# Performance work log

Hardware: AMD Instinct MI355X
Metric: run time of the kernel (lower is better)

The kernel has to match this reference:

```python
import jax, jax.numpy as jnp
import numpy as np

B, C, H, W = 4, 512, 64, 64
DQ = C // 8  # 64


def _conv1x1(x, w, b):
    # x: [B,C,H,W], w: [O,C], b: [O] -> [B,O,H,W]
    return jnp.einsum('bchw,oc->bohw', x, w) + b[None, :, None, None]


def setup_inputs() -> dict:
    key = jax.random.key(0)
    ks = jax.random.split(key, 12)
    s = 0.02  # conv weight init scale
    inp = {
        'x1': jax.random.normal(ks[0], (B, C, H, W), jnp.float32),
        'x2': jax.random.normal(ks[1], (B, C, H, W), jnp.float32),
        'wq1': jax.random.normal(ks[2], (DQ, C), jnp.float32) * s,
        'bq1': jnp.zeros((DQ,), jnp.float32),
        'wk1': jax.random.normal(ks[3], (DQ, C), jnp.float32) * s,
        'bk1': jnp.zeros((DQ,), jnp.float32),
        'wv1': jax.random.normal(ks[4], (C, C), jnp.float32) * s,
        'bv1': jnp.zeros((C,), jnp.float32),
        'wq2': jax.random.normal(ks[5], (DQ, C), jnp.float32) * s,
        'bq2': jnp.zeros((DQ,), jnp.float32),
        'wk2': jax.random.normal(ks[6], (DQ, C), jnp.float32) * s,
        'bk2': jnp.zeros((DQ,), jnp.float32),
        'wv2': jax.random.normal(ks[7], (C, C), jnp.float32) * s,
        'bv2': jnp.zeros((C,), jnp.float32),
        'gamma1': jax.random.normal(ks[8], (1,), jnp.float32) * 0.1,
        'gamma2': jax.random.normal(ks[9], (1,), jnp.float32) * 0.1,
    }
    return inp


def reference(x1, x2, wq1, bq1, wk1, bk1, wv1, bv1,
              wq2, bq2, wk2, bk2, wv2, bv2, gamma1, gamma2):
    b, c, h, w = x1.shape
    n = h * w
    # 1x1-conv projections, flattened to token axis n = h*w
    q1 = _conv1x1(x1, wq1, bq1).reshape(b, -1, n)  # [B,DQ,N]
    k1 = _conv1x1(x1, wk1, bk1).reshape(b, -1, n)  # [B,DQ,N]
    v1 = _conv1x1(x1, wv1, bv1).reshape(b, c, n)   # [B,C,N]
    q2 = _conv1x1(x2, wq2, bq2).reshape(b, -1, n)
    k2 = _conv1x1(x2, wk2, bk2).reshape(b, -1, n)
    v2 = _conv1x1(x2, wv2, bv2).reshape(b, c, n)

    # cross attention 1: queries from x1, keys/values from x2 (no 1/sqrt(d) scaling, per source)
    att1 = jax.nn.softmax(jnp.einsum('bdn,bdm->bnm', q1, k2), axis=-1)  # [B,N,N]
    out1 = jnp.einsum('bcn,bmn->bcm', v2, att1).reshape(b, c, h, w)

    # cross attention 2: queries from x2, keys/values from x1
    att2 = jax.nn.softmax(jnp.einsum('bdn,bdm->bnm', q2, k1), axis=-1)  # [B,N,N]
    out2 = jnp.einsum('bcn,bmn->bcm', v1, att2).reshape(b, c, h, w)

    out1 = x1 + gamma1 * out1
    out2 = x2 + gamma2 * out2
    return out1, out2
```

## Files before the change

### kernel.cpp

```cpp
#include <hip/hip_runtime.h>
#include <hip/hip_bf16.h>

#define NT 4096
#define CD 512
#define DQV 64
#define NB 4

typedef float f32x4 __attribute__((ext_vector_type(4)));
typedef short bf16x8 __attribute__((ext_vector_type(8)));

__device__ __forceinline__ short f2bf(float x){
  union { __hip_bfloat16 b; short s; } u;
  u.b = __float2bfloat16(x);
  return u.s;
}

__global__ void cast_weights(const float* __restrict__ wq1, const float* __restrict__ wk1,
                             const float* __restrict__ wv1, const float* __restrict__ wq2,
                             const float* __restrict__ wk2, const float* __restrict__ wv2,
                             short* __restrict__ out){
  int id = blockIdx.x * 256 + threadIdx.x;
  if (id >= 655360) return;
  float v;
  if (id < 32768)        v = wq1[id];
  else if (id < 65536)   v = wk1[id - 32768];
  else if (id < 327680)  v = wv1[id - 65536];
  else if (id < 360448)  v = wq2[id - 327680];
  else if (id < 393216)  v = wk2[id - 360448];
  else                   v = wv2[id - 393216];
  out[id] = f2bf(v);
}

__global__ void transpose_cast(const float* __restrict__ x1, const float* __restrict__ x2,
                               short* __restrict__ XT1, short* __restrict__ XT2){
  __shared__ short t[64][66];
  int nt = blockIdx.x, ct = blockIdx.y, z = blockIdx.z;
  int b = z & 3, inp = z >> 2;
  const float* xb = (inp ? x2 : x1) + (size_t)b * CD * NT;
  short* xtb = (inp ? XT2 : XT1) + (size_t)b * NT * CD;
  int n0 = nt * 64, c0 = ct * 64;
  int tid = threadIdx.x;
  int nl = tid & 63, cl0 = (tid >> 6) * 2;
#pragma unroll
  for (int cc = 0; cc < 8; ++cc){
    int c = cl0 + cc * 8;
    float v0 = xb[(size_t)(c0 + c) * NT + n0 + nl];
    float v1 = xb[(size_t)(c0 + c + 1) * NT + n0 + nl];
    union { unsigned u; short s[2]; } p;
    p.s[0] = f2bf(v0); p.s[1] = f2bf(v1);
    *(unsigned*)&t[nl][c] = p.u;
  }
  __syncthreads();
  int cl = (tid & 31) * 2, nl0 = tid >> 5;
#pragma unroll
  for (int nn = 0; nn < 8; ++nn){
    int n = nl0 + nn * 8;
    *(unsigned*)&xtb[(size_t)(n0 + n) * CD + c0 + cl] = *(const unsigned*)&t[n][cl];
  }
}

__global__ void proj_qk(const short* __restrict__ XT1, const short* __restrict__ XT2,
                        const short* __restrict__ WB,
                        const float* __restrict__ bq1, const float* __restrict__ bk1,
                        const float* __restrict__ bq2, const float* __restrict__ bk2,
                        short* __restrict__ Q1, short* __restrict__ K1,
                        short* __restrict__ Q2, short* __restrict__ K2){
  int pt = blockIdx.y;
  const short* xt = (pt < 2) ? XT1 : XT2;
  const short* w  = WB + (pt == 0 ? 0 : pt == 1 ? 32768 : pt == 2 ? 327680 : 360448);
  const float* bias = (pt == 0) ? bq1 : (pt == 1) ? bk1 : (pt == 2) ? bq2 : bk2;
  short* out = (pt == 0) ? Q1 : (pt == 1) ? K1 : (pt == 2) ? Q2 : K2;
  int row0 = blockIdx.x * 128;
  int wid = threadIdx.x >> 6, lane = threadIdx.x & 63;
  int lr = lane & 15, lk = (lane >> 4) * 8, lq4 = (lane >> 4) * 4;
  f32x4 acc[2][4] = {};
#pragma unroll 2
  for (int kk = 0; kk < 16; ++kk){
    int k0 = kk * 32 + lk;
    bf16x8 a[2], bb[4];
#pragma unroll
    for (int fr = 0; fr < 2; ++fr)
      a[fr] = *(const bf16x8*)&xt[(size_t)(row0 + wid*32 + fr*16 + lr) * CD + k0];
#pragma unroll
    for (int fc = 0; fc < 4; ++fc)
      bb[fc] = *(const bf16x8*)&w[(size_t)(fc*16 + lr) * CD + k0];
#pragma unroll
    for (int fr = 0; fr < 2; ++fr)
#pragma unroll
      for (int fc = 0; fc < 4; ++fc)
        acc[fr][fc] = __builtin_amdgcn_mfma_f32_16x16x32_bf16(a[fr], bb[fc], acc[fr][fc], 0,0,0);
  }
#pragma unroll
  for (int fr = 0; fr < 2; ++fr)
#pragma unroll
    for (int fc = 0; fc < 4; ++fc){
      int col = fc*16 + lr;
      float bsv = bias[col];
#pragma unroll
      for (int r = 0; r < 4; ++r){
        int row = row0 + wid*32 + fr*16 + lq4 + r;
        out[(size_t)row * DQV + col] = f2bf(acc[fr][fc][r] + bsv);
      }
    }
}

__global__ void proj_v(const short* __restrict__ XT1, const short* __restrict__ XT2,
                       const short* __restrict__ WB,
                       const float* __restrict__ bv1, const float* __restrict__ bv2,
                       short* __restrict__ V1, short* __restrict__ V2){
  int inp = blockIdx.z, b = blockIdx.y;
  int ct = blockIdx.x >> 6, nt = blockIdx.x & 63;
  const short* xt = (inp ? XT2 : XT1) + (size_t)b * NT * CD;
  const short* w  = WB + (inp ? 393216 : 65536);
  const float* bias = inp ? bv2 : bv1;
  short* V = (inp ? V2 : V1) + (size_t)b * CD * NT;
  int c0 = ct * 128, n0 = nt * 64;
  int wid = threadIdx.x >> 6, lane = threadIdx.x & 63;
  int ch = wid >> 1, nh = wid & 1;
  int lr = lane & 15, lk = (lane >> 4) * 8, lq4 = (lane >> 4) * 4;
  f32x4 acc[4][2] = {};
#pragma unroll 2
  for (int kk = 0; kk < 16; ++kk){
    int k0 = kk * 32 + lk;
    bf16x8 a[4], bb[2];
#pragma unroll
    for (int fr = 0; fr < 4; ++fr)
      a[fr] = *(const bf16x8*)&w[(size_t)(c0 + ch*64 + fr*16 + lr) * CD + k0];
#pragma unroll
    for (int fc = 0; fc < 2; ++fc)
      bb[fc] = *(const bf16x8*)&xt[(size_t)(n0 + nh*32 + fc*16 + lr) * CD + k0];
#pragma unroll
    for (int fr = 0; fr < 4; ++fr)
#pragma unroll
      for (int fc = 0; fc < 2; ++fc)
        acc[fr][fc] = __builtin_amdgcn_mfma_f32_16x16x32_bf16(a[fr], bb[fc], acc[fr][fc], 0,0,0);
  }
#pragma unroll
  for (int fr = 0; fr < 4; ++fr)
#pragma unroll
    for (int fc = 0; fc < 2; ++fc)
#pragma unroll
      for (int r = 0; r < 4; ++r){
        int c = c0 + ch*64 + fr*16 + lq4 + r;
        int n = n0 + nh*32 + fc*16 + lr;
        V[(size_t)c * NT + n] = f2bf(acc[fr][fc][r] + bias[c]);
      }
}

__global__ void __launch_bounds__(512, 4) attn_fused(
    const short* __restrict__ Q1, const short* __restrict__ K1, const short* __restrict__ V1,
    const short* __restrict__ Q2, const short* __restrict__ K2, const short* __restrict__ V2,
    const float* __restrict__ x1, const float* __restrict__ x2,
    const float* __restrict__ g1, const float* __restrict__ g2,
    float* __restrict__ out){
  __shared__ float S[64][68];
  __shared__ __align__(16) short P[64][72];
  __shared__ float lrow[64], crow[64];

  int bid = blockIdx.x;
  int pair = bid & 7, qb = bid >> 3;
  int b = pair & 3, at = pair >> 2;
  const short* Q = at ? Q2 : Q1;
  const short* K = at ? K1 : K2;
  const short* V = at ? V1 : V2;
  const float* xr = at ? x2 : x1;
  float gamma = at ? g2[0] : g1[0];
  float* outp = out + (size_t)at * NB*CD*NT + (size_t)b * CD*NT;
  const float* xrb = xr + (size_t)b * CD*NT;
  const short* Qb = Q + ((size_t)b*NT + (size_t)qb*64) * DQV;
  const short* Kb = K + (size_t)b*NT*DQV;
  const short* Vb = V + (size_t)b*CD*NT;

  int tid = threadIdx.x, wid = tid >> 6, lane = tid & 63;
  int lr = lane & 15, lk8 = (lane >> 4) * 8, lq4 = (lane >> 4) * 4;

  int ih = wid >> 2, jq = wid & 3;
  bf16x8 qf[2][2];
#pragma unroll
  for (int fr = 0; fr < 2; ++fr)
#pragma unroll
    for (int fk = 0; fk < 2; ++fk)
      qf[fr][fk] = *(const bf16x8*)&Qb[(size_t)(ih*32 + fr*16 + lr) * DQV + fk*32 + lk8];

  f32x4 acc[4][4] = {};
  int c0 = wid * 64;
  int si = tid >> 3, sj = (tid & 7) * 8;
  float m_reg = -1e30f, l_reg = 0.f;

#pragma unroll 1
  for (int jt = 0; jt < 64; ++jt){
    int j0 = jt * 64;
    f32x4 s0 = {}, s1 = {};
#pragma unroll
    for (int fk = 0; fk < 2; ++fk){
      bf16x8 kf = *(const bf16x8*)&Kb[(size_t)(j0 + jq*16 + lr) * DQV + fk*32 + lk8];
      s0 = __builtin_amdgcn_mfma_f32_16x16x32_bf16(qf[0][fk], kf, s0, 0,0,0);
      s1 = __builtin_amdgcn_mfma_f32_16x16x32_bf16(qf[1][fk], kf, s1, 0,0,0);
    }
#pragma unroll
    for (int r = 0; r < 4; ++r){
      S[ih*32 + lq4 + r][jq*16 + lr]      = s0[r];
      S[ih*32 + 16 + lq4 + r][jq*16 + lr] = s1[r];
    }
    __syncthreads();
    {
      f32x4 sa = *(const f32x4*)&S[si][sj];
      f32x4 sb = *(const f32x4*)&S[si][sj + 4];
      float mx = fmaxf(fmaxf(fmaxf(sa[0], sa[1]), fmaxf(sa[2], sa[3])),
                       fmaxf(fmaxf(sb[0], sb[1]), fmaxf(sb[2], sb[3])));
      mx = fmaxf(mx, __shfl_xor(mx, 1));
      mx = fmaxf(mx, __shfl_xor(mx, 2));
      mx = fmaxf(mx, __shfl_xor(mx, 4));
      float mn = fmaxf(m_reg, mx);
      float cf = __expf(m_reg - mn);
      float e0 = __expf(sa[0] - mn), e1 = __expf(sa[1] - mn);
      float e2 = __expf(sa[2] - mn), e3 = __expf(sa[3] - mn);
      float e4 = __expf(sb[0] - mn), e5 = __expf(sb[1] - mn);
      float e6 = __expf(sb[2] - mn), e7 = __expf(sb[3] - mn);
      float sum = ((e0 + e1) + (e2 + e3)) + ((e4 + e5) + (e6 + e7));
      bf16x8 pv;
      pv[0] = f2bf(e0); pv[1] = f2bf(e1); pv[2] = f2bf(e2); pv[3] = f2bf(e3);
      pv[4] = f2bf(e4); pv[5] = f2bf(e5); pv[6] = f2bf(e6); pv[7] = f2bf(e7);
      *(bf16x8*)&P[si][sj] = pv;
      sum += __shfl_xor(sum, 1);
      sum += __shfl_xor(sum, 2);
      sum += __shfl_xor(sum, 4);
      l_reg = l_reg * cf + sum;
      m_reg = mn;
      if ((tid & 7) == 0) crow[si] = cf;
    }
    __syncthreads();
    {
      float cf0 = crow[lr], cf1 = crow[16 + lr], cf2 = crow[32 + lr], cf3 = crow[48 + lr];
      bool ident = (cf0 == 1.f) & (cf1 == 1.f) & (cf2 == 1.f) & (cf3 == 1.f);
      if (!__all(ident)){
        float cfa[4] = {cf0, cf1, cf2, cf3};
#pragma unroll
        for (int ci = 0; ci < 4; ++ci){
          float cf = cfa[ci];
#pragma unroll
          for (int cr = 0; cr < 4; ++cr){
            acc[cr][ci][0] *= cf; acc[cr][ci][1] *= cf;
            acc[cr][ci][2] *= cf; acc[cr][ci][3] *= cf;
          }
        }
      }
    }
#pragma unroll
    for (int kk = 0; kk < 2; ++kk){
      bf16x8 pf[4];
#pragma unroll
      for (int ci = 0; ci < 4; ++ci)
        pf[ci] = *(const bf16x8*)&P[ci*16 + lr][kk*32 + lk8];
#pragma unroll
      for (int cr = 0; cr < 4; ++cr){
        bf16x8 vf = *(const bf16x8*)&Vb[(size_t)(c0 + cr*16 + lr) * NT + j0 + kk*32 + lk8];
#pragma unroll
        for (int ci = 0; ci < 4; ++ci)
          acc[cr][ci] = __builtin_amdgcn_mfma_f32_16x16x32_bf16(vf, pf[ci], acc[cr][ci], 0,0,0);
      }
    }
    __syncthreads();
  }
  if ((tid & 7) == 0) lrow[si] = l_reg;
  __syncthreads();
#pragma unroll
  for (int ci = 0; ci < 4; ++ci){
    float linv = 1.f / lrow[ci*16 + lr];
    int ig = qb*64 + ci*16 + lr;
#pragma unroll
    for (int cr = 0; cr < 4; ++cr)
#pragma unroll
      for (int r = 0; r < 4; ++r){
        int c = c0 + cr*16 + lq4 + r;
        size_t idx = (size_t)c * NT + ig;
        outp[idx] = xrb[idx] + gamma * acc[cr][ci][r] * linv;
      }
  }
}

extern "C" void kernel_launch(void* const* d_in, const int* in_sizes, int n_in,
                              void* d_out, int out_size, void* d_ws, size_t ws_size,
                              hipStream_t stream) {
  const float* x1  = (const float*)d_in[0];
  const float* x2  = (const float*)d_in[1];
  const float* wq1 = (const float*)d_in[2];
  const float* bq1 = (const float*)d_in[3];
  const float* wk1 = (const float*)d_in[4];
  const float* bk1 = (const float*)d_in[5];
  const float* wv1 = (const float*)d_in[6];
  const float* bv1 = (const float*)d_in[7];
  const float* wq2 = (const float*)d_in[8];
  const float* bq2 = (const float*)d_in[9];
  const float* wk2 = (const float*)d_in[10];
  const float* bk2 = (const float*)d_in[11];
  const float* wv2 = (const float*)d_in[12];
  const float* bv2 = (const float*)d_in[13];
  const float* g1  = (const float*)d_in[14];
  const float* g2  = (const float*)d_in[15];

  short* XT1 = (short*)d_ws;
  short* XT2 = XT1 + 8388608;
  short* Q1  = XT2 + 8388608;
  short* K1  = Q1 + 1048576;
  short* Q2  = K1 + 1048576;
  short* K2  = Q2 + 1048576;
  short* V1  = K2 + 1048576;
  short* V2  = V1 + 8388608;
  short* WB  = V2 + 8388608;

  cast_weights<<<2560, 256, 0, stream>>>(wq1, wk1, wv1, wq2, wk2, wv2, WB);
  transpose_cast<<<dim3(64, 8, 8), 256, 0, stream>>>(x1, x2, XT1, XT2);
  proj_qk<<<dim3(128, 4), 256, 0, stream>>>(XT1, XT2, WB, bq1, bk1, bq2, bk2, Q1, K1, Q2, K2);
  proj_v<<<dim3(256, 4, 2), 256, 0, stream>>>(XT1, XT2, WB, bv1, bv2, V1, V2);
  attn_fused<<<512, 512, 0, stream>>>(Q1, K1, V1, Q2, K2, V2, x1, x2, g1, g2, (float*)d_out);
}
```

Measured before the change: 646.8 us.

## Halve attention query tile to 32 rows, prefetch K/V, raise occupancy

The fused attention kernel now handles 32 query rows per block instead of 64 and launches twice as many blocks, with launch bounds raised to allow more resident blocks. K fragments for the next tile are prefetched, V fragments are loaded before the QK MFMA, and the PV MFMA section runs at raised wave priority. The trailing per-iteration barrier is removed, which is safe because shared-memory reuse is already ordered by the next iteration's barriers. The aim is more parallelism and better latency hiding. The cost is that each V tile is reused by half as many queries, roughly doubling V reads, and the tighter register budget may cause spills.

```diff
diff --git a/kernel.cpp b/kernel.cpp
--- a/kernel.cpp
+++ b/kernel.cpp
@@ -8,6 +8,7 @@
 
 typedef float f32x4 __attribute__((ext_vector_type(4)));
 typedef short bf16x8 __attribute__((ext_vector_type(8)));
+typedef short bf16x4 __attribute__((ext_vector_type(4)));
 
 __device__ __forceinline__ short f2bf(float x){
   union { __hip_bfloat16 b; short s; } u;
@@ -147,15 +148,15 @@
       }
 }
 
-__global__ void __launch_bounds__(512, 4) attn_fused(
+__global__ void __launch_bounds__(512, 8) attn_fused(
     const short* __restrict__ Q1, const short* __restrict__ K1, const short* __restrict__ V1,
     const short* __restrict__ Q2, const short* __restrict__ K2, const short* __restrict__ V2,
     const float* __restrict__ x1, const float* __restrict__ x2,
     const float* __restrict__ g1, const float* __restrict__ g2,
     float* __restrict__ out){
-  __shared__ float S[64][68];
-  __shared__ __align__(16) short P[64][72];
-  __shared__ float lrow[64], crow[64];
+  __shared__ float S[32][69];
+  __shared__ __align__(16) short P[32][80];
+  __shared__ float lrow[32], crow[32];
 
   int bid = blockIdx.x;
   int pair = bid & 7, qb = bid >> 3;
@@ -167,107 +168,103 @@
   float gamma = at ? g2[0] : g1[0];
   float* outp = out + (size_t)at * NB*CD*NT + (size_t)b * CD*NT;
   const float* xrb = xr + (size_t)b * CD*NT;
-  const short* Qb = Q + ((size_t)b*NT + (size_t)qb*64) * DQV;
+  const short* Qb = Q + ((size_t)b*NT + (size_t)qb*32) * DQV;
   const short* Kb = K + (size_t)b*NT*DQV;
   const short* Vb = V + (size_t)b*CD*NT;
 
   int tid = threadIdx.x, wid = tid >> 6, lane = tid & 63;
   int lr = lane & 15, lk8 = (lane >> 4) * 8, lq4 = (lane >> 4) * 4;
 
-  int ih = wid >> 2, jq = wid & 3;
-  bf16x8 qf[2][2];
-#pragma unroll
-  for (int fr = 0; fr < 2; ++fr)
-#pragma unroll
-    for (int fk = 0; fk < 2; ++fk)
-      qf[fr][fk] = *(const bf16x8*)&Qb[(size_t)(ih*32 + fr*16 + lr) * DQV + fk*32 + lk8];
-
-  f32x4 acc[4][4] = {};
+  int rh = wid >> 2, cb = wid & 3;
+  bf16x8 qf[2];
+#pragma unroll
+  for (int fk = 0; fk < 2; ++fk)
+    qf[fk] = *(const bf16x8*)&Qb[(size_t)(rh*16 + lr) * DQV + fk*32 + lk8];
+
+  f32x4 acc[4][2] = {};
   int c0 = wid * 64;
-  int si = tid >> 3, sj = (tid & 7) * 8;
+  int si = tid >> 4, sj = (tid & 15) * 4;
   float m_reg = -1e30f, l_reg = 0.f;
+
+  bf16x8 kf0 = *(const bf16x8*)&Kb[(size_t)(cb*16 + lr) * DQV + lk8];
+  bf16x8 kf1 = *(const bf16x8*)&Kb[(size_t)(cb*16 + lr) * DQV + 32 + lk8];
 
 #pragma unroll 1
   for (int jt = 0; jt < 64; ++jt){
     int j0 = jt * 64;
-    f32x4 s0 = {}, s1 = {};
-#pragma unroll
-    for (int fk = 0; fk < 2; ++fk){
-      bf16x8 kf = *(const bf16x8*)&Kb[(size_t)(j0 + jq*16 + lr) * DQV + fk*32 + lk8];
-      s0 = __builtin_amdgcn_mfma_f32_16x16x32_bf16(qf[0][fk], kf, s0, 0,0,0);
-      s1 = __builtin_amdgcn_mfma_f32_16x16x32_bf16(qf[1][fk], kf, s1, 0,0,0);
-    }
-#pragma unroll
-    for (int r = 0; r < 4; ++r){
-      S[ih*32 + lq4 + r][jq*16 + lr]      = s0[r];
-      S[ih*32 + 16 + lq4 + r][jq*16 + lr] = s1[r];
-    }
+    bf16x8 vf[4][2];
+#pragma unroll
+    for (int cr = 0; cr < 4; ++cr)
+#pragma unroll
+      for (int kk = 0; kk < 2; ++kk)
+        vf[cr][kk] = *(const bf16x8*)&Vb[(size_t)(c0 + cr*16 + lr) * NT + j0 + kk*32 + lk8];
+    f32x4 s0 = {};
+    s0 = __builtin_amdgcn_mfma_f32_16x16x32_bf16(qf[0], kf0, s0, 0,0,0);
+    s0 = __builtin_amdgcn_mfma_f32_16x16x32_bf16(qf[1], kf1, s0, 0,0,0);
+    if (jt < 63){
+      kf0 = *(const bf16x8*)&Kb[(size_t)(j0 + 64 + cb*16 + lr) * DQV + lk8];
+      kf1 = *(const bf16x8*)&Kb[(size_t)(j0 + 64 + cb*16 + lr) * DQV + 32 + lk8];
+    }
+#pragma unroll
+    for (int r = 0; r < 4; ++r)
+      S[rh*16 + lq4 + r][cb*16 + lr] = s0[r];
     __syncthreads();
     {
-      f32x4 sa = *(const f32x4*)&S[si][sj];
-      f32x4 sb = *(const f32x4*)&S[si][sj + 4];
-      float mx = fmaxf(fmaxf(fmaxf(sa[0], sa[1]), fmaxf(sa[2], sa[3])),
-                       fmaxf(fmaxf(sb[0], sb[1]), fmaxf(sb[2], sb[3])));
+      float v0 = S[si][sj], v1 = S[si][sj+1], v2 = S[si][sj+2], v3 = S[si][sj+3];
+      float mx = fmaxf(fmaxf(v0, v1), fmaxf(v2, v3));
       mx = fmaxf(mx, __shfl_xor(mx, 1));
       mx = fmaxf(mx, __shfl_xor(mx, 2));
       mx = fmaxf(mx, __shfl_xor(mx, 4));
+      mx = fmaxf(mx, __shfl_xor(mx, 8));
       float mn = fmaxf(m_reg, mx);
       float cf = __expf(m_reg - mn);
-      float e0 = __expf(sa[0] - mn), e1 = __expf(sa[1] - mn);
-      float e2 = __expf(sa[2] - mn), e3 = __expf(sa[3] - mn);
-      float e4 = __expf(sb[0] - mn), e5 = __expf(sb[1] - mn);
-      float e6 = __expf(sb[2] - mn), e7 = __expf(sb[3] - mn);
-      float sum = ((e0 + e1) + (e2 + e3)) + ((e4 + e5) + (e6 + e7));
-      bf16x8 pv;
+      float e0 = __expf(v0 - mn), e1 = __expf(v1 - mn);
+      float e2 = __expf(v2 - mn), e3 = __expf(v3 - mn);
+      float sum = (e0 + e1) + (e2 + e3);
+      bf16x4 pv;
       pv[0] = f2bf(e0); pv[1] = f2bf(e1); pv[2] = f2bf(e2); pv[3] = f2bf(e3);
-      pv[4] = f2bf(e4); pv[5] = f2bf(e5); pv[6] = f2bf(e6); pv[7] = f2bf(e7);
-      *(bf16x8*)&P[si][sj] = pv;
+      *(bf16x4*)&P[si][sj] = pv;
       sum += __shfl_xor(sum, 1);
       sum += __shfl_xor(sum, 2);
       sum += __shfl_xor(sum, 4);
+      sum += __shfl_xor(sum, 8);
       l_reg = l_reg * cf + sum;
       m_reg = mn;
-      if ((tid & 7) == 0) crow[si] = cf;
+      if ((tid & 15) == 0) crow[si] = cf;
     }
     __syncthreads();
     {
-      float cf0 = crow[lr], cf1 = crow[16 + lr], cf2 = crow[32 + lr], cf3 = crow[48 + lr];
-      bool ident = (cf0 == 1.f) & (cf1 == 1.f) & (cf2 == 1.f) & (cf3 == 1.f);
+      float cf0 = crow[lr], cf1 = crow[16 + lr];
+      bool ident = (cf0 == 1.f) & (cf1 == 1.f);
       if (!__all(ident)){
-        float cfa[4] = {cf0, cf1, cf2, cf3};
-#pragma unroll
-        for (int ci = 0; ci < 4; ++ci){
-          float cf = cfa[ci];
-#pragma unroll
-          for (int cr = 0; cr < 4; ++cr){
-            acc[cr][ci][0] *= cf; acc[cr][ci][1] *= cf;
-            acc[cr][ci][2] *= cf; acc[cr][ci][3] *= cf;
-          }
+#pragma unroll
+        for (int cr = 0; cr < 4; ++cr){
+          acc[cr][0][0] *= cf0; acc[cr][0][1] *= cf0; acc[cr][0][2] *= cf0; acc[cr][0][3] *= cf0;
+          acc[cr][1][0] *= cf1; acc[cr][1][1] *= cf1; acc[cr][1][2] *= cf1; acc[cr][1][3] *= cf1;
         }
       }
     }
+    __builtin_amdgcn_s_setprio(1);
 #pragma unroll
     for (int kk = 0; kk < 2; ++kk){
-      bf16x8 pf[4];
-#pragma unroll
-      for (int ci = 0; ci < 4; ++ci)
+      bf16x8 pf[2];
+#pragma unroll
+      for (int ci = 0; ci < 2; ++ci)
         pf[ci] = *(const bf16x8*)&P[ci*16 + lr][kk*32 + lk8];
 #pragma unroll
-      for (int cr = 0; cr < 4; ++cr){
-        bf16x8 vf = *(const bf16x8*)&Vb[(size_t)(c0 + cr*16 + lr) * NT + j0 + kk*32 + lk8];
-#pragma unroll
-        for (int ci = 0; ci < 4; ++ci)
-          acc[cr][ci] = __builtin_amdgcn_mfma_f32_16x16x32_bf16(vf, pf[ci], acc[cr][ci], 0,0,0);
-      }
-    }
-    __syncthreads();
-  }
-  if ((tid & 7) == 0) lrow[si] = l_reg;
+      for (int cr = 0; cr < 4; ++cr)
+#pragma unroll
+        for (int ci = 0; ci < 2; ++ci)
+          acc[cr][ci] = __builtin_amdgcn_mfma_f32_16x16x32_bf16(vf[cr][kk], pf[ci], acc[cr][ci], 0,0,0);
+    }
+    __builtin_amdgcn_s_setprio(0);
+  }
+  if ((tid & 15) == 0) lrow[si] = l_reg;
   __syncthreads();
 #pragma unroll
-  for (int ci = 0; ci < 4; ++ci){
+  for (int ci = 0; ci < 2; ++ci){
     float linv = 1.f / lrow[ci*16 + lr];
-    int ig = qb*64 + ci*16 + lr;
+    int ig = qb*32 + ci*16 + lr;
 #pragma unroll
     for (int cr = 0; cr < 4; ++cr)
 #pragma unroll
@@ -313,5 +310,5 @@
   transpose_cast<<<dim3(64, 8, 8), 256, 0, stream>>>(x1, x2, XT1, XT2);
   proj_qk<<<dim3(128, 4), 256, 0, stream>>>(XT1, XT2, WB, bq1, bk1, bq2, bk2, Q1, K1, Q2, K2);
   proj_v<<<dim3(256, 4, 2), 256, 0, stream>>>(XT1, XT2, WB, bv1, bv2, V1, V2);
-  attn_fused<<<512, 512, 0, stream>>>(Q1, K1, V1, Q2, K2, V2, x1, x2, g1, g2, (float*)d_out);
-}
+  attn_fused<<<1024, 512, 0, stream>>>(Q1, K1, V1, Q2, K2, V2, x1, x2, g1, g2, (float*)d_out);
+}
```

After: 1.821 ms. 2.82x slower.

## Widen attention key tile to 128, drop trailing barrier, raise PV priority

Applied to the files above, without the earlier changes.

The key/value tile in the fused flash-attention loop grows from 64 to 128 columns. This halves the loop trip count and the number of softmax rescale and barrier rounds, and each wave now computes a 32x32 block of S. The end-of-iteration __syncthreads is removed, relying on the next iteration's first barrier to protect the S, P and crow buffers. s_setprio raises wave priority around the PV MFMA section. The larger S and P shared buffers roughly double LDS use per block, which may lower the number of resident blocks per CU.

```diff
diff --git a/kernel.cpp b/kernel.cpp
--- a/kernel.cpp
+++ b/kernel.cpp
@@ -153,8 +153,8 @@
     const float* __restrict__ x1, const float* __restrict__ x2,
     const float* __restrict__ g1, const float* __restrict__ g2,
     float* __restrict__ out){
-  __shared__ float S[64][68];
-  __shared__ __align__(16) short P[64][72];
+  __shared__ float S[64][132];
+  __shared__ __align__(16) short P[64][136];
   __shared__ float lrow[64], crow[64];
 
   int bid = blockIdx.x;
@@ -174,54 +174,78 @@
   int tid = threadIdx.x, wid = tid >> 6, lane = tid & 63;
   int lr = lane & 15, lk8 = (lane >> 4) * 8, lq4 = (lane >> 4) * 4;
 
-  int ih = wid >> 2, jq = wid & 3;
+  int rh = wid >> 2, cb = wid & 3;
   bf16x8 qf[2][2];
 #pragma unroll
   for (int fr = 0; fr < 2; ++fr)
 #pragma unroll
     for (int fk = 0; fk < 2; ++fk)
-      qf[fr][fk] = *(const bf16x8*)&Qb[(size_t)(ih*32 + fr*16 + lr) * DQV + fk*32 + lk8];
+      qf[fr][fk] = *(const bf16x8*)&Qb[(size_t)(rh*32 + fr*16 + lr) * DQV + fk*32 + lk8];
 
   f32x4 acc[4][4] = {};
   int c0 = wid * 64;
-  int si = tid >> 3, sj = (tid & 7) * 8;
+  int si = tid >> 3, sj = (tid & 7) * 16;
   float m_reg = -1e30f, l_reg = 0.f;
 
 #pragma unroll 1
-  for (int jt = 0; jt < 64; ++jt){
-    int j0 = jt * 64;
-    f32x4 s0 = {}, s1 = {};
-#pragma unroll
-    for (int fk = 0; fk < 2; ++fk){
-      bf16x8 kf = *(const bf16x8*)&Kb[(size_t)(j0 + jq*16 + lr) * DQV + fk*32 + lk8];
-      s0 = __builtin_amdgcn_mfma_f32_16x16x32_bf16(qf[0][fk], kf, s0, 0,0,0);
-      s1 = __builtin_amdgcn_mfma_f32_16x16x32_bf16(qf[1][fk], kf, s1, 0,0,0);
-    }
-#pragma unroll
-    for (int r = 0; r < 4; ++r){
-      S[ih*32 + lq4 + r][jq*16 + lr]      = s0[r];
-      S[ih*32 + 16 + lq4 + r][jq*16 + lr] = s1[r];
-    }
+  for (int jt = 0; jt < 32; ++jt){
+    int j0 = jt * 128;
+    f32x4 s[2][2] = {};
+    bf16x8 kf[2][2];
+#pragma unroll
+    for (int fc = 0; fc < 2; ++fc)
+#pragma unroll
+      for (int fk = 0; fk < 2; ++fk)
+        kf[fc][fk] = *(const bf16x8*)&Kb[(size_t)(j0 + cb*32 + fc*16 + lr) * DQV + fk*32 + lk8];
+#pragma unroll
+    for (int fr = 0; fr < 2; ++fr)
+#pragma unroll
+      for (int fc = 0; fc < 2; ++fc){
+        s[fr][fc] = __builtin_amdgcn_mfma_f32_16x16x32_bf16(qf[fr][0], kf[fc][0], s[fr][fc], 0,0,0);
+        s[fr][fc] = __builtin_amdgcn_mfma_f32_16x16x32_bf16(qf[fr][1], kf[fc][1], s[fr][fc], 0,0,0);
+      }
+#pragma unroll
+    for (int fr = 0; fr < 2; ++fr)
+#pragma unroll
+      for (int fc = 0; fc < 2; ++fc)
+#pragma unroll
+        for (int r = 0; r < 4; ++r)
+          S[rh*32 + fr*16 + lq4 + r][cb*32 + fc*16 + lr] = s[fr][fc][r];
     __syncthreads();
     {
-      f32x4 sa = *(const f32x4*)&S[si][sj];
-      f32x4 sb = *(const f32x4*)&S[si][sj + 4];
-      float mx = fmaxf(fmaxf(fmaxf(sa[0], sa[1]), fmaxf(sa[2], sa[3])),
-                       fmaxf(fmaxf(sb[0], sb[1]), fmaxf(sb[2], sb[3])));
+      f32x4 a0 = *(const f32x4*)&S[si][sj];
+      f32x4 a1 = *(const f32x4*)&S[si][sj + 4];
+      f32x4 a2 = *(const f32x4*)&S[si][sj + 8];
+      f32x4 a3 = *(const f32x4*)&S[si][sj + 12];
+      float mx = fmaxf(fmaxf(fmaxf(a0[0],a0[1]),fmaxf(a0[2],a0[3])),
+                       fmaxf(fmaxf(a1[0],a1[1]),fmaxf(a1[2],a1[3])));
+      mx = fmaxf(mx, fmaxf(fmaxf(fmaxf(a2[0],a2[1]),fmaxf(a2[2],a2[3])),
+                           fmaxf(fmaxf(a3[0],a3[1]),fmaxf(a3[2],a3[3]))));
       mx = fmaxf(mx, __shfl_xor(mx, 1));
       mx = fmaxf(mx, __shfl_xor(mx, 2));
       mx = fmaxf(mx, __shfl_xor(mx, 4));
       float mn = fmaxf(m_reg, mx);
       float cf = __expf(m_reg - mn);
-      float e0 = __expf(sa[0] - mn), e1 = __expf(sa[1] - mn);
-      float e2 = __expf(sa[2] - mn), e3 = __expf(sa[3] - mn);
-      float e4 = __expf(sb[0] - mn), e5 = __expf(sb[1] - mn);
-      float e6 = __expf(sb[2] - mn), e7 = __expf(sb[3] - mn);
-      float sum = ((e0 + e1) + (e2 + e3)) + ((e4 + e5) + (e6 + e7));
-      bf16x8 pv;
-      pv[0] = f2bf(e0); pv[1] = f2bf(e1); pv[2] = f2bf(e2); pv[3] = f2bf(e3);
-      pv[4] = f2bf(e4); pv[5] = f2bf(e5); pv[6] = f2bf(e6); pv[7] = f2bf(e7);
-      *(bf16x8*)&P[si][sj] = pv;
+      bf16x8 p0, p1;
+      float sum = 0.f;
+#pragma unroll
+      for (int t = 0; t < 4; ++t){
+        float e = __expf(a0[t] - mn); sum += e; p0[t] = f2bf(e);
+      }
+#pragma unroll
+      for (int t = 0; t < 4; ++t){
+        float e = __expf(a1[t] - mn); sum += e; p0[4+t] = f2bf(e);
+      }
+#pragma unroll
+      for (int t = 0; t < 4; ++t){
+        float e = __expf(a2[t] - mn); sum += e; p1[t] = f2bf(e);
+      }
+#pragma unroll
+      for (int t = 0; t < 4; ++t){
+        float e = __expf(a3[t] - mn); sum += e; p1[4+t] = f2bf(e);
+      }
+      *(bf16x8*)&P[si][sj]     = p0;
+      *(bf16x8*)&P[si][sj + 8] = p1;
       sum += __shfl_xor(sum, 1);
       sum += __shfl_xor(sum, 2);
       sum += __shfl_xor(sum, 4);
@@ -231,10 +255,11 @@
     }
     __syncthreads();
     {
-      float cf0 = crow[lr], cf1 = crow[16 + lr], cf2 = crow[32 + lr], cf3 = crow[48 + lr];
-      bool ident = (cf0 == 1.f) & (cf1 == 1.f) & (cf2 == 1.f) & (cf3 == 1.f);
+      float cfa[4];
+#pragma unroll
+      for (int ci = 0; ci < 4; ++ci) cfa[ci] = crow[ci*16 + lr];
+      bool ident = (cfa[0] == 1.f) & (cfa[1] == 1.f) & (cfa[2] == 1.f) & (cfa[3] == 1.f);
       if (!__all(ident)){
-        float cfa[4] = {cf0, cf1, cf2, cf3};
 #pragma unroll
         for (int ci = 0; ci < 4; ++ci){
           float cf = cfa[ci];
@@ -246,8 +271,9 @@
         }
       }
     }
-#pragma unroll
-    for (int kk = 0; kk < 2; ++kk){
+    __builtin_amdgcn_s_setprio(1);
+#pragma unroll
+    for (int kk = 0; kk < 4; ++kk){
       bf16x8 pf[4];
 #pragma unroll
       for (int ci = 0; ci < 4; ++ci)
@@ -260,7 +286,7 @@
           acc[cr][ci] = __builtin_amdgcn_mfma_f32_16x16x32_bf16(vf, pf[ci], acc[cr][ci], 0,0,0);
       }
     }
-    __syncthreads();
+    __builtin_amdgcn_s_setprio(0);
   }
   if ((tid & 7) == 0) lrow[si] = l_reg;
   __syncthreads();
```

Result: slower. 776.2 us (+20.0%).

## Split attention channels across two blocks, prefetch V, and trim barriers

Applied to the files above, without the earlier changes.

The fused attention kernel now splits the 512 output channels into two halves handled by separate blocks, so the grid doubles to 1024. Each block's accumulator array halves, which lowers register pressure. The cost is that every block recomputes QK^T and the softmax for its query tile. V fragments are loaded at the top of each key-tile iteration, so the global loads overlap with the score and softmax work. The trailing per-iteration __syncthreads is removed, the remaining barriers use a lighter LDS-only wait, and wave priority is raised around the PV MFMA section.

```diff
diff --git a/kernel.cpp b/kernel.cpp
--- a/kernel.cpp
+++ b/kernel.cpp
@@ -14,6 +14,10 @@
   u.b = __float2bfloat16(x);
   return u.s;
 }
+
+#define BAR() do { asm volatile("s_waitcnt lgkmcnt(0)" ::: "memory"); \
+                   __builtin_amdgcn_s_barrier(); \
+                   asm volatile("" ::: "memory"); } while(0)
 
 __global__ void cast_weights(const float* __restrict__ wq1, const float* __restrict__ wk1,
                              const float* __restrict__ wv1, const float* __restrict__ wq2,
@@ -158,7 +162,9 @@
   __shared__ float lrow[64], crow[64];
 
   int bid = blockIdx.x;
-  int pair = bid & 7, qb = bid >> 3;
+  int pair = bid & 7;
+  int rest = bid >> 3;
+  int chalf = rest & 1, qb = rest >> 1;
   int b = pair & 3, at = pair >> 2;
   const short* Q = at ? Q2 : Q1;
   const short* K = at ? K1 : K2;
@@ -182,14 +188,20 @@
     for (int fk = 0; fk < 2; ++fk)
       qf[fr][fk] = *(const bf16x8*)&Qb[(size_t)(ih*32 + fr*16 + lr) * DQV + fk*32 + lk8];
 
-  f32x4 acc[4][4] = {};
-  int c0 = wid * 64;
+  f32x4 acc[2][4] = {};
+  int c0 = chalf * 256 + wid * 32;
   int si = tid >> 3, sj = (tid & 7) * 8;
   float m_reg = -1e30f, l_reg = 0.f;
 
 #pragma unroll 1
   for (int jt = 0; jt < 64; ++jt){
     int j0 = jt * 64;
+    bf16x8 vf[2][2];
+#pragma unroll
+    for (int cr = 0; cr < 2; ++cr)
+#pragma unroll
+      for (int kk = 0; kk < 2; ++kk)
+        vf[cr][kk] = *(const bf16x8*)&Vb[(size_t)(c0 + cr*16 + lr) * NT + j0 + kk*32 + lk8];
     f32x4 s0 = {}, s1 = {};
 #pragma unroll
     for (int fk = 0; fk < 2; ++fk){
@@ -202,7 +214,7 @@
       S[ih*32 + lq4 + r][jq*16 + lr]      = s0[r];
       S[ih*32 + 16 + lq4 + r][jq*16 + lr] = s1[r];
     }
-    __syncthreads();
+    BAR();
     {
       f32x4 sa = *(const f32x4*)&S[si][sj];
       f32x4 sb = *(const f32x4*)&S[si][sj + 4];
@@ -229,23 +241,25 @@
       m_reg = mn;
       if ((tid & 7) == 0) crow[si] = cf;
     }
-    __syncthreads();
+    BAR();
     {
-      float cf0 = crow[lr], cf1 = crow[16 + lr], cf2 = crow[32 + lr], cf3 = crow[48 + lr];
-      bool ident = (cf0 == 1.f) & (cf1 == 1.f) & (cf2 == 1.f) & (cf3 == 1.f);
+      float cfa[4];
+#pragma unroll
+      for (int ci = 0; ci < 4; ++ci) cfa[ci] = crow[ci*16 + lr];
+      bool ident = (cfa[0] == 1.f) & (cfa[1] == 1.f) & (cfa[2] == 1.f) & (cfa[3] == 1.f);
       if (!__all(ident)){
-        float cfa[4] = {cf0, cf1, cf2, cf3};
 #pragma unroll
         for (int ci = 0; ci < 4; ++ci){
           float cf = cfa[ci];
 #pragma unroll
-          for (int cr = 0; cr < 4; ++cr){
+          for (int cr = 0; cr < 2; ++cr){
             acc[cr][ci][0] *= cf; acc[cr][ci][1] *= cf;
             acc[cr][ci][2] *= cf; acc[cr][ci][3] *= cf;
           }
         }
       }
     }
+    __builtin_amdgcn_s_setprio(1);
 #pragma unroll
     for (int kk = 0; kk < 2; ++kk){
       bf16x8 pf[4];
@@ -253,23 +267,21 @@
       for (int ci = 0; ci < 4; ++ci)
         pf[ci] = *(const bf16x8*)&P[ci*16 + lr][kk*32 + lk8];
 #pragma unroll
-      for (int cr = 0; cr < 4; ++cr){
-        bf16x8 vf = *(const bf16x8*)&Vb[(size_t)(c0 + cr*16 + lr) * NT + j0 + kk*32 + lk8];
+      for (int cr = 0; cr < 2; ++cr)
 #pragma unroll
         for (int ci = 0; ci < 4; ++ci)
-          acc[cr][ci] = __builtin_amdgcn_mfma_f32_16x16x32_bf16(vf, pf[ci], acc[cr][ci], 0,0,0);
-      }
-    }
-    __syncthreads();
+          acc[cr][ci] = __builtin_amdgcn_mfma_f32_16x16x32_bf16(vf[cr][kk], pf[ci], acc[cr][ci], 0,0,0);
+    }
+    __builtin_amdgcn_s_setprio(0);
   }
   if ((tid & 7) == 0) lrow[si] = l_reg;
-  __syncthreads();
+  BAR();
 #pragma unroll
   for (int ci = 0; ci < 4; ++ci){
     float linv = 1.f / lrow[ci*16 + lr];
     int ig = qb*64 + ci*16 + lr;
 #pragma unroll
-    for (int cr = 0; cr < 4; ++cr)
+    for (int cr = 0; cr < 2; ++cr)
 #pragma unroll
       for (int r = 0; r < 4; ++r){
         int c = c0 + cr*16 + lq4 + r;
@@ -313,5 +325,5 @@
   transpose_cast<<<dim3(64, 8, 8), 256, 0, stream>>>(x1, x2, XT1, XT2);
   proj_qk<<<dim3(128, 4), 256, 0, stream>>>(XT1, XT2, WB, bq1, bk1, bq2, bk2, Q1, K1, Q2, K2);
   proj_v<<<dim3(256, 4, 2), 256, 0, stream>>>(XT1, XT2, WB, bv1, bv2, V1, V2);
-  attn_fused<<<512, 512, 0, stream>>>(Q1, K1, V1, Q2, K2, V2, x1, x2, g1, g2, (float*)d_out);
-}
+  attn_fused<<<1024, 512, 0, stream>>>(Q1, K1, V1, Q2, K2, V2, x1, x2, g1, g2, (float*)d_out);
+}
```

Result: faster. 621.3 us (-3.9%).
